# Performance work log

Hardware: AMD Instinct MI355X
Metric: run time of the kernel (lower is better)

Reference implementation:

```python
import jax, jax.numpy as jnp
import numpy as np

VOCAB = 6
EPS = 1e-12


def _conv1d_same(x, w):
    # x: [B, Cin, L], w: [Cout, Cin, K] (odd K) -> [B, Cout, L]
    k = w.shape[-1]
    return jax.lax.conv_general_dilated(
        x, w, window_strides=(1,), padding=[(k // 2, k // 2)],
        dimension_numbers=("NCH", "OIH", "NCH"))


def setup_inputs() -> dict:
    key = jax.random.key(0)
    k1, k2, k3, k4 = jax.random.split(key, 4)
    B, L = 32, 2048
    Cin, Cout = VOCAB - 1, 256
    return {
        "input_ids": jax.random.randint(k1, (B, L), 0, VOCAB, dtype=jnp.int64),
        "attention_mask": jnp.ones((B, L), dtype=jnp.float32),
        "W3": jax.random.normal(k2, (Cout, Cin, 3), dtype=jnp.float32) * 0.1,
        "W5": jax.random.normal(k3, (Cout, Cin, 5), dtype=jnp.float32) * 0.1,
        "W7": jax.random.normal(k4, (Cout, Cin, 7), dtype=jnp.float32) * 0.1,
        "ln_gamma": jnp.ones((768,), dtype=jnp.float32),
        "ln_beta": jnp.zeros((768,), dtype=jnp.float32),
    }


def reference(input_ids, attention_mask, W3, W5, W7, ln_gamma, ln_beta):
    # One-hot over vocab, drop last class (padding token) -> [B, Cin, L]
    oh = jax.nn.one_hot(input_ids, VOCAB, dtype=jnp.float32)[:, :, : VOCAB - 1]
    x = jnp.transpose(oh, (0, 2, 1))  # [B, Cin, L]
    # Multi-kernel Conv1d, concat along channel dim -> [B, 768, L]
    h = jnp.concatenate([_conv1d_same(x, W3), _conv1d_same(x, W5), _conv1d_same(x, W7)], axis=1)
    # Zero out padded positions
    h = h * attention_mask[:, None, :]
    # [B, L, 768] then LayerNorm over last dim
    h = jnp.transpose(h, (0, 2, 1))
    mu = jnp.mean(h, axis=-1, keepdims=True)
    var = jnp.mean(jnp.square(h - mu), axis=-1, keepdims=True)
    out = (h - mu) * jax.lax.rsqrt(var + EPS) * ln_gamma + ln_beta
    return out  # dropout p=0.0 / eval mode -> identity
```

## Files before the change

kernel.cpp:

```cpp
#include <hip/hip_runtime.h>
#include <math.h>

namespace {

constexpr int kL       = 2048;
constexpr int kThreads = 512;
constexpr int kBlkPos  = 128;
constexpr int kPosPerWave = 16;

typedef float    vfloat4 __attribute__((ext_vector_type(4)));
typedef _Float16 half4   __attribute__((ext_vector_type(4)));

template <int CTRL, int RM, bool BC>
__device__ __forceinline__ float dpp_acc(float x) {
    const int y = __builtin_amdgcn_update_dpp(0, __float_as_int(x), CTRL, RM, 0xF, BC);
    return x + __int_as_float(y);
}

__device__ __forceinline__ float wave_sum(float x) {
    x = dpp_acc<0xB1,  0xF, true >(x);
    x = dpp_acc<0x4E,  0xF, true >(x);
    x = dpp_acc<0x124, 0xF, true >(x);
    x = dpp_acc<0x128, 0xF, true >(x);
    x = dpp_acc<0x142, 0xA, false>(x);
    x = dpp_acc<0x143, 0xC, false>(x);
    return __int_as_float(__builtin_amdgcn_readlane(__float_as_int(x), 63));
}

__device__ __forceinline__ int wrow(int t, int c) {
    return (c == 5) ? 75 : (t * 5 + c);
}

__global__ __launch_bounds__(kThreads, 4)
void cnn_emb_ln(const int*   __restrict__ ids,
                const float* __restrict__ mask,
                const float* __restrict__ W3,
                const float* __restrict__ W5,
                const float* __restrict__ W7,
                const float* __restrict__ gamma,
                const float* __restrict__ beta,
                float*       __restrict__ out)
{
    __shared__ half4 sW[76][64];

    const int tid  = threadIdx.x;
    const int lane = tid & 63;
    const int wave = tid >> 6;

    _Float16* sWh = reinterpret_cast<_Float16*>(sW);
    if (tid < 256) sWh[75 * 256 + tid] = (_Float16)0.f;

    {
        const float4* v4 = reinterpret_cast<const float4*>(W3);
        for (int i = tid; i < 960; i += kThreads) {
            const float4 v = v4[i];
            const float f[4] = {v.x, v.y, v.z, v.w};
            #pragma unroll
            for (int j = 0; j < 4; ++j) {
                const int e = 4 * i + j, o = e / 15, r = e % 15;
                sWh[((r % 3) * 5 + (r / 3)) * 256 + o] = (_Float16)f[j];
            }
        }
    }
    {
        const float4* v4 = reinterpret_cast<const float4*>(W5);
        for (int i = tid; i < 1600; i += kThreads) {
            const float4 v = v4[i];
            const float f[4] = {v.x, v.y, v.z, v.w};
            #pragma unroll
            for (int j = 0; j < 4; ++j) {
                const int e = 4 * i + j, o = e / 25, r = e % 25;
                sWh[((3 + r % 5) * 5 + (r / 5)) * 256 + o] = (_Float16)f[j];
            }
        }
    }
    {
        const float4* v4 = reinterpret_cast<const float4*>(W7);
        for (int i = tid; i < 2240; i += kThreads) {
            const float4 v = v4[i];
            const float f[4] = {v.x, v.y, v.z, v.w};
            #pragma unroll
            for (int j = 0; j < 4; ++j) {
                const int e = 4 * i + j, o = e / 35, r = e % 35;
                sWh[((8 + r % 7) * 5 + (r / 7)) * 256 + o] = (_Float16)f[j];
            }
        }
    }

    const int p0 = blockIdx.x * kBlkPos + wave * kPosPerWave;
    const int l0 = p0 & (kL - 1);

    int myc = 5;
    if (lane < kPosPerWave + 6) {
        const int lp = l0 - 3 + lane;
        if (lp >= 0 && lp < kL) {
            const int v = ids[p0 - 3 + lane];
            myc = (v < 5) ? v : 5;
        }
    }
    float mym = 0.f;
    if (lane < kPosPerWave) mym = mask[p0 + lane];

    float ga[3][4], be[3][4];
    #pragma unroll
    for (int g = 0; g < 3; ++g) {
        const float4 gg = *reinterpret_cast<const float4*>(gamma + g * 256 + 4 * lane);
        const float4 bb = *reinterpret_cast<const float4*>(beta  + g * 256 + 4 * lane);
        ga[g][0] = gg.x; ga[g][1] = gg.y; ga[g][2] = gg.z; ga[g][3] = gg.w;
        be[g][0] = bb.x; be[g][1] = bb.y; be[g][2] = bb.z; be[g][3] = bb.w;
    }

    __syncthreads();

    #pragma unroll
    for (int i = 0; i < kPosPerWave; ++i) {
        int c[7];
        #pragma unroll
        for (int j = 0; j < 7; ++j) c[j] = __builtin_amdgcn_readlane(myc, i + j);
        const float m = __int_as_float(__builtin_amdgcn_readlane(__float_as_int(mym), i));

        const half4 a3 =  sW[wrow(0, c[2])][lane] + sW[wrow(1, c[3])][lane]
                       +  sW[wrow(2, c[4])][lane];
        const half4 a5 = (sW[wrow(3, c[1])][lane] + sW[wrow(4, c[2])][lane])
                       + (sW[wrow(5, c[3])][lane] + sW[wrow(6, c[4])][lane])
                       +  sW[wrow(7, c[5])][lane];
        const half4 a7 = ((sW[wrow( 8, c[0])][lane] + sW[wrow( 9, c[1])][lane])
                       +  (sW[wrow(10, c[2])][lane] + sW[wrow(11, c[3])][lane]))
                       + ((sW[wrow(12, c[4])][lane] + sW[wrow(13, c[5])][lane])
                       +   sW[wrow(14, c[6])][lane]);

        const float h3[4] = {(float)a3.x, (float)a3.y, (float)a3.z, (float)a3.w};
        const float h5[4] = {(float)a5.x, (float)a5.y, (float)a5.z, (float)a5.w};
        const float h7[4] = {(float)a7.x, (float)a7.y, (float)a7.z, (float)a7.w};

        float s = ((h3[0] + h3[1]) + (h3[2] + h3[3]))
                + ((h5[0] + h5[1]) + (h5[2] + h5[3]))
                + ((h7[0] + h7[1]) + (h7[2] + h7[3]));
        float ss = h3[0] * h3[0];
        ss = fmaf(h3[1], h3[1], ss); ss = fmaf(h3[2], h3[2], ss); ss = fmaf(h3[3], h3[3], ss);
        ss = fmaf(h5[0], h5[0], ss); ss = fmaf(h5[1], h5[1], ss); ss = fmaf(h5[2], h5[2], ss);
        ss = fmaf(h5[3], h5[3], ss); ss = fmaf(h7[0], h7[0], ss); ss = fmaf(h7[1], h7[1], ss);
        ss = fmaf(h7[2], h7[2], ss); ss = fmaf(h7[3], h7[3], ss);

        const float s_tot  = wave_sum(s);
        const float ss_tot = wave_sum(ss);

        const float inv_n = 1.0f / 768.0f;
        const float mu  = m * s_tot * inv_n;
        const float ex2 = (m * m) * ss_tot * inv_n;
        const float var = fmaxf(ex2 - mu * mu, 0.0f);
        const float rs  = rsqrtf(var + 1e-12f);
        const float aa  = m * rs;
        const float cc  = -mu * rs;

        float* o = out + (size_t)(p0 + i) * 768 + 4 * lane;

        vfloat4 r;
        r.x = fmaf(fmaf(h3[0], aa, cc), ga[0][0], be[0][0]);
        r.y = fmaf(fmaf(h3[1], aa, cc), ga[0][1], be[0][1]);
        r.z = fmaf(fmaf(h3[2], aa, cc), ga[0][2], be[0][2]);
        r.w = fmaf(fmaf(h3[3], aa, cc), ga[0][3], be[0][3]);
        *reinterpret_cast<vfloat4*>(o) = r;

        r.x = fmaf(fmaf(h5[0], aa, cc), ga[1][0], be[1][0]);
        r.y = fmaf(fmaf(h5[1], aa, cc), ga[1][1], be[1][1]);
        r.z = fmaf(fmaf(h5[2], aa, cc), ga[1][2], be[1][2]);
        r.w = fmaf(fmaf(h5[3], aa, cc), ga[1][3], be[1][3]);
        *reinterpret_cast<vfloat4*>(o + 256) = r;

        r.x = fmaf(fmaf(h7[0], aa, cc), ga[2][0], be[2][0]);
        r.y = fmaf(fmaf(h7[1], aa, cc), ga[2][1], be[2][1]);
        r.z = fmaf(fmaf(h7[2], aa, cc), ga[2][2], be[2][2]);
        r.w = fmaf(fmaf(h7[3], aa, cc), ga[2][3], be[2][3]);
        *reinterpret_cast<vfloat4*>(o + 512) = r;
    }
}

}

extern "C" void kernel_launch(void* const* d_in, const int* in_sizes, int n_in,
                              void* d_out, int out_size, void* d_ws, size_t ws_size,
                              hipStream_t stream) {
    const int*   ids   = (const int*)  d_in[0];
    const float* mask  = (const float*)d_in[1];
    const float* W3    = (const float*)d_in[2];
    const float* W5    = (const float*)d_in[3];
    const float* W7    = (const float*)d_in[4];
    const float* gamma = (const float*)d_in[5];
    const float* beta  = (const float*)d_in[6];
    float*       out   = (float*)d_out;

    const int npos = in_sizes[0];
    const int grid = npos / kBlkPos;

    hipLaunchKernelGGL(cnn_emb_ln, dim3(grid), dim3(kThreads), 0, stream,
                       ids, mask, W3, W5, W7, gamma, beta, out);
}
```

Measured before the change: 42.14 us.

## Halve per-block positions, raise occupancy, use fdot2 stats and interleaved reductions

Halves the positions per wave and per block, doubling the grid, and raises the launch-bounds occupancy hint from 4 to 8 blocks. The per-position sum and sum of squares now come from packed fp16 dot2 instructions instead of converting to fp32 first. The two wave reductions are interleaved so their DPP steps can overlap. Gamma and beta are held in fp16 registers to cut register pressure. The trade-off is that every block still rebuilds the full weight table in shared memory, and twice as many blocks now repeat that setup, while gamma/beta lose precision in fp16.

Measured after the change: 43.72 us. 3.7% more time.

```diff
diff --git a/kernel.cpp b/kernel.cpp
--- a/kernel.cpp
+++ b/kernel.cpp
@@ -5,33 +5,44 @@
 
 constexpr int kL       = 2048;
 constexpr int kThreads = 512;
-constexpr int kBlkPos  = 128;
-constexpr int kPosPerWave = 16;
+constexpr int kBlkPos  = 64;
+constexpr int kPosPerWave = 8;
 
 typedef float    vfloat4 __attribute__((ext_vector_type(4)));
 typedef _Float16 half4   __attribute__((ext_vector_type(4)));
+typedef _Float16 half2   __attribute__((ext_vector_type(2)));
 
 template <int CTRL, int RM, bool BC>
-__device__ __forceinline__ float dpp_acc(float x) {
-    const int y = __builtin_amdgcn_update_dpp(0, __float_as_int(x), CTRL, RM, 0xF, BC);
-    return x + __int_as_float(y);
-}
-
-__device__ __forceinline__ float wave_sum(float x) {
-    x = dpp_acc<0xB1,  0xF, true >(x);
-    x = dpp_acc<0x4E,  0xF, true >(x);
-    x = dpp_acc<0x124, 0xF, true >(x);
-    x = dpp_acc<0x128, 0xF, true >(x);
-    x = dpp_acc<0x142, 0xA, false>(x);
-    x = dpp_acc<0x143, 0xC, false>(x);
-    return __int_as_float(__builtin_amdgcn_readlane(__float_as_int(x), 63));
-}
+__device__ __forceinline__ float dpp_step(float x) {
+    return __int_as_float(__builtin_amdgcn_update_dpp(0, __float_as_int(x), CTRL, RM, 0xF, BC));
+}
+
+__device__ __forceinline__ void wave_sum2(float& x, float& y) {
+    float tx, ty;
+    tx = dpp_step<0xB1,  0xF, true >(x);  ty = dpp_step<0xB1,  0xF, true >(y);
+    x += tx;                              y += ty;
+    tx = dpp_step<0x4E,  0xF, true >(x);  ty = dpp_step<0x4E,  0xF, true >(y);
+    x += tx;                              y += ty;
+    tx = dpp_step<0x124, 0xF, true >(x);  ty = dpp_step<0x124, 0xF, true >(y);
+    x += tx;                              y += ty;
+    tx = dpp_step<0x128, 0xF, true >(x);  ty = dpp_step<0x128, 0xF, true >(y);
+    x += tx;                              y += ty;
+    tx = dpp_step<0x142, 0xA, false>(x);  ty = dpp_step<0x142, 0xA, false>(y);
+    x += tx;                              y += ty;
+    tx = dpp_step<0x143, 0xC, false>(x);  ty = dpp_step<0x143, 0xC, false>(y);
+    x += tx;                              y += ty;
+    x = __int_as_float(__builtin_amdgcn_readlane(__float_as_int(x), 63));
+    y = __int_as_float(__builtin_amdgcn_readlane(__float_as_int(y), 63));
+}
+
+__device__ __forceinline__ half2 vlo(half4 v) { return __builtin_shufflevector(v, v, 0, 1); }
+__device__ __forceinline__ half2 vhi(half4 v) { return __builtin_shufflevector(v, v, 2, 3); }
 
 __device__ __forceinline__ int wrow(int t, int c) {
     return (c == 5) ? 75 : (t * 5 + c);
 }
 
-__global__ __launch_bounds__(kThreads, 4)
+__global__ __launch_bounds__(kThreads, 8)
 void cnn_emb_ln(const int*   __restrict__ ids,
                 const float* __restrict__ mask,
                 const float* __restrict__ W3,
@@ -101,16 +112,19 @@
     float mym = 0.f;
     if (lane < kPosPerWave) mym = mask[p0 + lane];
 
-    float ga[3][4], be[3][4];
+    half4 gh[3], bh[3];
     #pragma unroll
     for (int g = 0; g < 3; ++g) {
         const float4 gg = *reinterpret_cast<const float4*>(gamma + g * 256 + 4 * lane);
         const float4 bb = *reinterpret_cast<const float4*>(beta  + g * 256 + 4 * lane);
-        ga[g][0] = gg.x; ga[g][1] = gg.y; ga[g][2] = gg.z; ga[g][3] = gg.w;
-        be[g][0] = bb.x; be[g][1] = bb.y; be[g][2] = bb.z; be[g][3] = bb.w;
+        gh[g] = half4{(_Float16)gg.x, (_Float16)gg.y, (_Float16)gg.z, (_Float16)gg.w};
+        bh[g] = half4{(_Float16)bb.x, (_Float16)bb.y, (_Float16)bb.z, (_Float16)bb.w};
     }
 
     __syncthreads();
+
+    const half2 ones = {(_Float16)1.f, (_Float16)1.f};
+    const float inv_n = 1.0f / 768.0f;
 
     #pragma unroll
     for (int i = 0; i < kPosPerWave; ++i) {
@@ -129,25 +143,23 @@
                        + ((sW[wrow(12, c[4])][lane] + sW[wrow(13, c[5])][lane])
                        +   sW[wrow(14, c[6])][lane]);
 
-        const float h3[4] = {(float)a3.x, (float)a3.y, (float)a3.z, (float)a3.w};
-        const float h5[4] = {(float)a5.x, (float)a5.y, (float)a5.z, (float)a5.w};
-        const float h7[4] = {(float)a7.x, (float)a7.y, (float)a7.z, (float)a7.w};
-
-        float s = ((h3[0] + h3[1]) + (h3[2] + h3[3]))
-                + ((h5[0] + h5[1]) + (h5[2] + h5[3]))
-                + ((h7[0] + h7[1]) + (h7[2] + h7[3]));
-        float ss = h3[0] * h3[0];
-        ss = fmaf(h3[1], h3[1], ss); ss = fmaf(h3[2], h3[2], ss); ss = fmaf(h3[3], h3[3], ss);
-        ss = fmaf(h5[0], h5[0], ss); ss = fmaf(h5[1], h5[1], ss); ss = fmaf(h5[2], h5[2], ss);
-        ss = fmaf(h5[3], h5[3], ss); ss = fmaf(h7[0], h7[0], ss); ss = fmaf(h7[1], h7[1], ss);
-        ss = fmaf(h7[2], h7[2], ss); ss = fmaf(h7[3], h7[3], ss);
-
-        const float s_tot  = wave_sum(s);
-        const float ss_tot = wave_sum(ss);
-
-        const float inv_n = 1.0f / 768.0f;
-        const float mu  = m * s_tot * inv_n;
-        const float ex2 = (m * m) * ss_tot * inv_n;
+        float s = __builtin_amdgcn_fdot2(vlo(a3), ones, 0.f, false);
+        s = __builtin_amdgcn_fdot2(vhi(a3), ones, s, false);
+        s = __builtin_amdgcn_fdot2(vlo(a5), ones, s, false);
+        s = __builtin_amdgcn_fdot2(vhi(a5), ones, s, false);
+        s = __builtin_amdgcn_fdot2(vlo(a7), ones, s, false);
+        s = __builtin_amdgcn_fdot2(vhi(a7), ones, s, false);
+        float q = __builtin_amdgcn_fdot2(vlo(a3), vlo(a3), 0.f, false);
+        q = __builtin_amdgcn_fdot2(vhi(a3), vhi(a3), q, false);
+        q = __builtin_amdgcn_fdot2(vlo(a5), vlo(a5), q, false);
+        q = __builtin_amdgcn_fdot2(vhi(a5), vhi(a5), q, false);
+        q = __builtin_amdgcn_fdot2(vlo(a7), vlo(a7), q, false);
+        q = __builtin_amdgcn_fdot2(vhi(a7), vhi(a7), q, false);
+
+        wave_sum2(s, q);
+
+        const float mu  = m * s * inv_n;
+        const float ex2 = (m * m) * q * inv_n;
         const float var = fmaxf(ex2 - mu * mu, 0.0f);
         const float rs  = rsqrtf(var + 1e-12f);
         const float aa  = m * rs;
@@ -156,22 +168,22 @@
         float* o = out + (size_t)(p0 + i) * 768 + 4 * lane;
 
         vfloat4 r;
-        r.x = fmaf(fmaf(h3[0], aa, cc), ga[0][0], be[0][0]);
-        r.y = fmaf(fmaf(h3[1], aa, cc), ga[0][1], be[0][1]);
-        r.z = fmaf(fmaf(h3[2], aa, cc), ga[0][2], be[0][2]);
-        r.w = fmaf(fmaf(h3[3], aa, cc), ga[0][3], be[0][3]);
+        r.x = fmaf(fmaf((float)a3.x, aa, cc), (float)gh[0].x, (float)bh[0].x);
+        r.y = fmaf(fmaf((float)a3.y, aa, cc), (float)gh[0].y, (float)bh[0].y);
+        r.z = fmaf(fmaf((float)a3.z, aa, cc), (float)gh[0].z, (float)bh[0].z);
+        r.w = fmaf(fmaf((float)a3.w, aa, cc), (float)gh[0].w, (float)bh[0].w);
         *reinterpret_cast<vfloat4*>(o) = r;
 
-        r.x = fmaf(fmaf(h5[0], aa, cc), ga[1][0], be[1][0]);
-        r.y = fmaf(fmaf(h5[1], aa, cc), ga[1][1], be[1][1]);
-        r.z = fmaf(fmaf(h5[2], aa, cc), ga[1][2], be[1][2]);
-        r.w = fmaf(fmaf(h5[3], aa, cc), ga[1][3], be[1][3]);
+        r.x = fmaf(fmaf((float)a5.x, aa, cc), (float)gh[1].x, (float)bh[1].x);
+        r.y = fmaf(fmaf((float)a5.y, aa, cc), (float)gh[1].y, (float)bh[1].y);
+        r.z = fmaf(fmaf((float)a5.z, aa, cc), (float)gh[1].z, (float)bh[1].z);
+        r.w = fmaf(fmaf((float)a5.w, aa, cc), (float)gh[1].w, (float)bh[1].w);
         *reinterpret_cast<vfloat4*>(o + 256) = r;
 
-        r.x = fmaf(fmaf(h7[0], aa, cc), ga[2][0], be[2][0]);
-        r.y = fmaf(fmaf(h7[1], aa, cc), ga[2][1], be[2][1]);
-        r.z = fmaf(fmaf(h7[2], aa, cc), ga[2][2], be[2][2]);
-        r.w = fmaf(fmaf(h7[3], aa, cc), ga[2][3], be[2][3]);
+        r.x = fmaf(fmaf((float)a7.x, aa, cc), (float)gh[2].x, (float)bh[2].x);
+        r.y = fmaf(fmaf((float)a7.y, aa, cc), (float)gh[2].y, (float)bh[2].y);
+        r.z = fmaf(fmaf((float)a7.z, aa, cc), (float)gh[2].z, (float)bh[2].z);
+        r.w = fmaf(fmaf((float)a7.w, aa, cc), (float)gh[2].w, (float)bh[2].w);
         *reinterpret_cast<vfloat4*>(o + 512) = r;
     }
 }
```
